# Kernel tuning notes

Measured on AMD Instinct MI355X. Metric: run time of the kernel, lower is better.

The kernel has to match this reference:

```python
import math
import jax, jax.numpy as jnp
import numpy as np

_GELU_C = math.sqrt(2.0 / math.pi)

def _gelu_tanh(x):
    return 0.5 * x * (1.0 + jnp.tanh(_GELU_C * (x + 0.044715 * x * x * x)))

def _l2_normalize(v, eps=1e-12):
    # matches F.normalize: v / max(||v||, eps)
    n = jnp.sqrt(jnp.sum(v * v, axis=-1, keepdims=True))
    return v / jnp.maximum(n, eps)

def setup_inputs() -> dict:
    key = jax.random.key(0)
    k1, k2, k3 = jax.random.split(key, 3)
    B, T, D = 8, 2048, 1024
    x = jax.random.normal(k1, (B, T, D), dtype=jnp.float32)
    # nn.Parameter initial values from the module
    log_alpha = jnp.asarray(math.log(math.exp(0.5) - 1.0), dtype=jnp.float32)
    log_sigma = jnp.asarray(math.log(1.0), dtype=jnp.float32)
    return {"x": x, "log_alpha": log_alpha, "log_sigma": log_sigma}

def reference(x, log_alpha, log_sigma):
    B, T, D = x.shape
    alpha = jax.nn.softplus(log_alpha)
    sigma = jax.nn.softplus(log_sigma)
    scale = 1.0 / math.sqrt(D)
    # full strictly-past causal attention (triu with diagonal=0 masks self too)
    sim = jnp.einsum('btd,bsd->bts', x, x) * scale            # [B,T,T]
    causal = jnp.triu(jnp.ones((T, T), dtype=bool), k=0)      # True = masked
    sim = jnp.where(causal[None], -jnp.inf, sim)
    # NaN-safe masked softmax: fully-masked rows (t=0) -> all zeros,
    # matching torch softmax + nan_to_num(nan=0.0)
    m = jnp.max(sim, axis=-1, keepdims=True)
    m_safe = jnp.where(jnp.isfinite(m), m, 0.0)
    e = jnp.exp(sim - m_safe)                                 # -inf -> 0
    denom = jnp.sum(e, axis=-1, keepdims=True)
    attn = jnp.where(denom > 0, e / jnp.where(denom > 0, denom, 1.0), 0.0)
    context = jnp.einsum('bts,bsd->btd', attn, x)             # [B,T,D]
    cos_sim = jnp.sum(_l2_normalize(x) * _l2_normalize(context), axis=-1)  # [B,T]
    novelty = jnp.clip(1.0 - cos_sim, 0.0, 2.0) / 2.0
    novelty = jnp.nan_to_num(novelty, nan=1.0)
    gate = 1.0 + alpha * jnp.tanh(sigma * novelty[..., None])
    return _gelu_tanh(x * gate)
```

## Files before the change

### kernel.cpp

```cpp
#include <hip/hip_runtime.h>
#include <math.h>

#define TN 2048
#define DN 1024

typedef __attribute__((ext_vector_type(8))) _Float16 half8;
typedef __attribute__((ext_vector_type(4))) _Float16 half4v;
typedef __attribute__((ext_vector_type(4))) float f32x4;

__device__ __forceinline__ f32x4 mfma16(half8 a, half8 b, f32x4 c) {
  return __builtin_amdgcn_mfma_f32_16x16x32_f16(a, b, c, 0, 0, 0);
}

#define BAR_LDS()  asm volatile("s_waitcnt lgkmcnt(0)\ns_barrier" ::: "memory")
#define WAITVM0()  asm volatile("s_waitcnt vmcnt(0)" ::: "memory")

__device__ __forceinline__ int img_off(int key, int f) {
  const int kg = key >> 2;
  const int p  = ((kg & 1) << 2) | (kg >> 1);
  return (f >> 4) * 512 + p * 64 + (key & 3) * 16 + (f & 15);
}

__global__ __launch_bounds__(256) void convert_x(const float* __restrict__ x,
                                                 _Float16* __restrict__ w) {
  const long long gid = (long long)blockIdx.x * 256 + threadIdx.x;
  const long long e   = gid * 8;
  const int bt   = (int)(e >> 15);
  const int et   = (int)(e & 32767);
  const int f16b = et >> 9;
  const int p    = (et >> 6) & 7;
  const int row  = (et >> 4) & 3;
  const int col0 = et & 15;
  const int kg   = ((p & 3) << 1) | (p >> 2);
  const int key  = kg * 4 + row;
  const size_t xoff = ((size_t)bt * 32 + key) * DN + f16b * 16 + col0;
  float4 u0 = *(const float4*)(x + xoff);
  float4 u1 = *(const float4*)(x + xoff + 4);
  half8 h = {(_Float16)u0.x, (_Float16)u0.y, (_Float16)u0.z, (_Float16)u0.w,
             (_Float16)u1.x, (_Float16)u1.y, (_Float16)u1.z, (_Float16)u1.w};
  *(half8*)(w + e) = h;
}

#define ISSUE4(T, O0, O1, O2, O3)                                             \
  asm volatile("ds_read_b64_tr_b16 %0, %4 offset:" O0 "\n\t"                  \
               "ds_read_b64_tr_b16 %1, %4 offset:" O1 "\n\t"                  \
               "ds_read_b64_tr_b16 %2, %4 offset:" O2 "\n\t"                  \
               "ds_read_b64_tr_b16 %3, %4 offset:" O3                         \
               : "=&v"(T[0]), "=&v"(T[1]), "=&v"(T[2]), "=&v"(T[3])           \
               : "v"(ab));

#define MFMA2(T, CT0, CT1)                                                    \
  {                                                                           \
    half8 bf0 = __builtin_shufflevector(T[0], T[1], 0, 1, 2, 3, 4, 5, 6, 7);  \
    half8 bf1 = __builtin_shufflevector(T[2], T[3], 0, 1, 2, 3, 4, 5, 6, 7);  \
    oacc[CT0] = mfma16(aP, bf0, oacc[CT0]);                                   \
    oacc[CT1] = mfma16(aP, bf1, oacc[CT1]);                                   \
  }

template <bool WS>
__global__ __launch_bounds__(512, 4)
void attn_gate(const float* __restrict__ x, const _Float16* __restrict__ wsx,
               const float* __restrict__ pla, const float* __restrict__ pls,
               float* __restrict__ out) {
  __shared__ _Float16 Kbuf[32768];
  __shared__ _Float16 Sred[8][16][40];
  __shared__ float l_s[16], gate_s[16];

  const int tid = threadIdx.x;
  const int w   = tid >> 6;
  const int l   = tid & 63;
  const int lr  = l & 15;
  const int lg  = l >> 4;
  const int kq  = w;

  const int b   = blockIdx.x & 7;
  const int q16 = 127 - (blockIdx.x >> 3);
  const int qbase = q16 * 16;
  const int nkt   = (qbase + 14) / 32 + 1;

  const float alpha = log1pf(expf(pla[0]));
  const float sigma = log1pf(expf(pls[0]));

  const float* xb = x + (size_t)b * TN * DN;
  float*       ob = out + (size_t)b * TN * DN;

  const int kg0 = lr >> 2;
  const int bk0 = ((((kg0 & 1) << 2) | (kg0 >> 1)) << 6) + (lr & 3) * 16 + (lg & 1) * 8;
  const int kg1 = 4 + (lr >> 2);
  const int bk1 = ((((kg1 & 1) << 2) | (kg1 >> 1)) << 6) + (lr & 3) * 16 + (lg & 1) * 8;

  auto STAGE = [&](int t) {
    if constexpr (WS) {
      const _Float16* tn = wsx + (size_t)(b * 64 + t) * 32768;
#pragma unroll
      for (int i = 0; i < 8; ++i)
        __builtin_amdgcn_global_load_lds(
            (const __attribute__((address_space(1))) void*)(tn + w * 4096 + i * 512 + l * 8),
            (__attribute__((address_space(3))) void*)(&Kbuf[w * 4096 + i * 512]), 16, 0, 0);
    } else {
      const int skey = tid >> 4, sc = tid & 15;
      const float* kp = xb + (size_t)(t * 32 + skey) * DN + sc * 4;
#pragma unroll
      for (int j = 0; j < 16; ++j) {
        const int f = sc * 4 + 64 * j;
        float4 v = *(const float4*)(kp + 64 * j);
        half4v h = {(_Float16)v.x, (_Float16)v.y, (_Float16)v.z, (_Float16)v.w};
        *(half4v*)&Kbuf[img_off(skey, f)] = h;
      }
    }
  };

  STAGE(0);

  half8 qf[4];
  if constexpr (WS) {
    const _Float16* qtile = wsx + (size_t)(b * 64 + (q16 >> 1)) * 32768;
    const int qrow = (q16 & 1) * 16 + lr;
    const int g0   = qrow >> 2;
    const int qp   = (((g0 & 1) << 2) | (g0 >> 1)) * 64 + (qrow & 3) * 16 + (lg & 1) * 8;
#pragma unroll
    for (int s = 0; s < 4; ++s)
      qf[s] = *(const half8*)&qtile[(kq * 8 + s * 2 + (lg >> 1)) * 512 + qp];
  } else {
#pragma unroll
    for (int s = 0; s < 4; ++s) {
      const float* qp = xb + (size_t)(qbase + lr) * DN + kq * 128 + s * 32 + lg * 8;
      float4 a = ((const float4*)qp)[0];
      float4 c = ((const float4*)qp)[1];
      half8 h;
      h[0]=(_Float16)a.x; h[1]=(_Float16)a.y; h[2]=(_Float16)a.z; h[3]=(_Float16)a.w;
      h[4]=(_Float16)c.x; h[5]=(_Float16)c.y; h[6]=(_Float16)c.z; h[7]=(_Float16)c.w;
      qf[s] = h;
    }
  }

  f32x4 oacc[8];
#pragma unroll
  for (int ct = 0; ct < 8; ++ct) oacc[ct] = f32x4{0.f, 0.f, 0.f, 0.f};
  float l0 = 0.0f;

  if constexpr (!WS) __syncthreads();

  for (int t = 0; t < nkt; ++t) {
    if constexpr (WS) WAITVM0();

    {
      f32x4 sA = f32x4{0.f,0.f,0.f,0.f};
      f32x4 sB = f32x4{0.f,0.f,0.f,0.f};
#pragma unroll
      for (int s = 0; s < 4; ++s) {
        const int base = (kq * 8 + s * 2 + (lg >> 1)) * 512;
        half8 bf0 = *(const half8*)&Kbuf[base + bk0];
        half8 bf1 = *(const half8*)&Kbuf[base + bk1];
        sA = mfma16(bf0, qf[s], sA);
        sB = mfma16(bf1, qf[s], sB);
      }
      half4v hA = {(_Float16)sA[0], (_Float16)sA[1], (_Float16)sA[2], (_Float16)sA[3]};
      half4v hB = {(_Float16)sB[0], (_Float16)sB[1], (_Float16)sB[2], (_Float16)sB[3]};
      *(half4v*)&Sred[kq][lr][lg * 4]      = hA;
      *(half4v*)&Sred[kq][lr][16 + lg * 4] = hB;
    }
    BAR_LDS();

    {
      half8 r0 = *(const half8*)&Sred[0][lr][lg * 8];
      half8 r1 = *(const half8*)&Sred[1][lr][lg * 8];
      half8 r2 = *(const half8*)&Sred[2][lr][lg * 8];
      half8 r3 = *(const half8*)&Sred[3][lr][lg * 8];
      half8 r4 = *(const half8*)&Sred[4][lr][lg * 8];
      half8 r5 = *(const half8*)&Sred[5][lr][lg * 8];
      half8 r6 = *(const half8*)&Sred[6][lr][lg * 8];
      half8 r7 = *(const half8*)&Sred[7][lr][lg * 8];
      half8 sum = ((r0 + r1) + (r2 + r3)) + ((r4 + r5) + (r6 + r7));

      const bool mt = (t == nkt - 1);
      const int  gb = 32 * t + lg * 8;
      half8 aP;
#pragma unroll
      for (int j = 0; j < 8; ++j) {
        float p = __expf((float)sum[j] * 0.03125f);
        if (mt && (gb + j >= qbase + lr)) p = 0.0f;
        l0 += p;
        aP[j] = (_Float16)p;
      }

      const uint32_t ab = (uint32_t)(uintptr_t)(void*)&Kbuf[w * 4096 + l * 4];
      asm volatile("s_waitcnt lgkmcnt(0)" ::: "memory");
      __builtin_amdgcn_sched_barrier(0);
      half4v t0[4], t1[4];
      ISSUE4(t0, "0", "512", "1024", "1536");
      ISSUE4(t1, "2048", "2560", "3072", "3584");
      asm volatile("s_waitcnt lgkmcnt(4)" ::: "memory");
      __builtin_amdgcn_sched_barrier(0);
      MFMA2(t0, 0, 1);
      ISSUE4(t0, "4096", "4608", "5120", "5632");
      asm volatile("s_waitcnt lgkmcnt(4)" ::: "memory");
      __builtin_amdgcn_sched_barrier(0);
      MFMA2(t1, 2, 3);
      ISSUE4(t1, "6144", "6656", "7168", "7680");
      asm volatile("s_waitcnt lgkmcnt(4)" ::: "memory");
      __builtin_amdgcn_sched_barrier(0);
      MFMA2(t0, 4, 5);
      asm volatile("s_waitcnt lgkmcnt(0)" ::: "memory");
      __builtin_amdgcn_sched_barrier(0);
      MFMA2(t1, 6, 7);
    }

    if (t + 1 < nkt) {
      if constexpr (!WS) __syncthreads();
      STAGE(t + 1);
    }
    BAR_LDS();
  }

  {
    float lt = l0 + __shfl_xor(l0, 16);
    lt += __shfl_xor(lt, 32);
    if (w == 0 && lg == 0) l_s[lr] = lt;
  }

  {
    float* ered = (float*)&Sred[0][0][0];
#pragma unroll
    for (int j = 0; j < 4; ++j) {
      const int row = lg * 4 + j;
      const float* xr = xb + (size_t)(qbase + row) * DN + w * 128 + lr;
      float a1 = 0.f, a2 = 0.f, a3 = 0.f;
#pragma unroll
      for (int ct = 0; ct < 8; ++ct) {
        const float xv = xr[ct * 16];
        const float ov = oacc[ct][j];
        a1 += xv * ov; a2 += xv * xv; a3 += ov * ov;
      }
#pragma unroll
      for (int d = 1; d < 16; d <<= 1) {
        a1 += __shfl_xor(a1, d);
        a2 += __shfl_xor(a2, d);
        a3 += __shfl_xor(a3, d);
      }
      if (lr == 0) {
        float* e = ered + (row * 8 + w) * 4;
        e[0] = a1; e[1] = a2; e[2] = a3;
      }
    }
  }
  __syncthreads();
  if (tid < 16) {
    const float* ered = (const float*)&Sred[0][0][0];
    float SxO = 0.f, Sxx = 0.f, SOO = 0.f;
#pragma unroll
    for (int wv = 0; wv < 8; ++wv) {
      const float* e = ered + (tid * 8 + wv) * 4;
      SxO += e[0]; Sxx += e[1]; SOO += e[2];
    }
    const float lden = l_s[tid];
    float cosv = 0.0f;
    if (lden > 0.0f) {
      const float nx = fmaxf(sqrtf(Sxx), 1e-12f);
      const float nc = fmaxf(sqrtf(SOO) / lden, 1e-12f);
      cosv = (SxO / lden) / (nx * nc);
    }
    float nov = fminf(fmaxf(1.0f - cosv, 0.0f), 2.0f) * 0.5f;
    gate_s[tid] = 1.0f + alpha * tanhf(sigma * nov);
  }
  __syncthreads();
  {
#pragma unroll
    for (int j = 0; j < 4; ++j) {
      const int row = lg * 4 + j;
      const float g = gate_s[row];
      const float* xr = xb + (size_t)(qbase + row) * DN + w * 128 + lr;
      float* orow     = ob + (size_t)(qbase + row) * DN + w * 128 + lr;
#pragma unroll
      for (int ct = 0; ct < 8; ++ct) {
        const float z = xr[ct * 16] * g;
        const float u = 0.7978845608028654f * (z + 0.044715f * z * z * z);
        orow[ct * 16] = 0.5f * z * (1.0f + tanhf(u));
      }
    }
  }
}

extern "C" void kernel_launch(void* const* d_in, const int* in_sizes, int n_in,
                              void* d_out, int out_size, void* d_ws, size_t ws_size,
                              hipStream_t stream) {
  const float* x  = (const float*)d_in[0];
  const float* la = (const float*)d_in[1];
  const float* ls = (const float*)d_in[2];
  float* out = (float*)d_out;
  const size_t need = (size_t)8 * 64 * 32768 * 2;
  if (ws_size >= need) {
    convert_x<<<dim3(8192), dim3(256), 0, stream>>>(x, (_Float16*)d_ws);
    attn_gate<true><<<dim3(1024), dim3(512), 0, stream>>>(
        x, (const _Float16*)d_ws, la, ls, out);
  } else {
    attn_gate<false><<<dim3(1024), dim3(512), 0, stream>>>(
        x, (const _Float16*)nullptr, la, ls, out);
  }
}
```

Before: 194.8 us.

## Load QK^T key fragments directly from global with one-tile register prefetch

In the workspace path, the key fragments for the score MFMA are now read directly from global memory into registers and prefetched one tile ahead, instead of being read from LDS after a full vmcnt(0) wait. The LDS-staged copy is still used only for the PV step, gated by a partial vmcnt(8) wait so the register prefetch loads can stay in flight. The Sred row pitch is also padded from 40 to 44 halves to change LDS bank mapping. The aim is to overlap global latency with compute and take traffic off LDS, at the cost of more VGPRs (16 half8 registers) and duplicated global reads that rely on cache hits.

```diff
diff --git a/kernel.cpp b/kernel.cpp
--- a/kernel.cpp
+++ b/kernel.cpp
@@ -13,7 +13,6 @@
 }
 
 #define BAR_LDS()  asm volatile("s_waitcnt lgkmcnt(0)\ns_barrier" ::: "memory")
-#define WAITVM0()  asm volatile("s_waitcnt vmcnt(0)" ::: "memory")
 
 __device__ __forceinline__ int img_off(int key, int f) {
   const int kg = key >> 2;
@@ -63,7 +62,7 @@
                const float* __restrict__ pla, const float* __restrict__ pls,
                float* __restrict__ out) {
   __shared__ _Float16 Kbuf[32768];
-  __shared__ _Float16 Sred[8][16][40];
+  __shared__ _Float16 Sred[8][16][44];
   __shared__ float l_s[16], gate_s[16];
 
   const int tid = threadIdx.x;
@@ -89,9 +88,11 @@
   const int kg1 = 4 + (lr >> 2);
   const int bk1 = ((((kg1 & 1) << 2) | (kg1 >> 1)) << 6) + (lr & 3) * 16 + (lg & 1) * 8;
 
+  const _Float16* wsb = WS ? (wsx + (size_t)b * 64 * 32768) : nullptr;
+
   auto STAGE = [&](int t) {
     if constexpr (WS) {
-      const _Float16* tn = wsx + (size_t)(b * 64 + t) * 32768;
+      const _Float16* tn = wsb + (size_t)t * 32768;
 #pragma unroll
       for (int i = 0; i < 8; ++i)
         __builtin_amdgcn_global_load_lds(
@@ -114,7 +115,7 @@
 
   half8 qf[4];
   if constexpr (WS) {
-    const _Float16* qtile = wsx + (size_t)(b * 64 + (q16 >> 1)) * 32768;
+    const _Float16* qtile = wsb + (size_t)(q16 >> 1) * 32768;
     const int qrow = (q16 & 1) * 16 + lr;
     const int g0   = qrow >> 2;
     const int qp   = (((g0 & 1) << 2) | (g0 >> 1)) * 64 + (qrow & 3) * 16 + (lg & 1) * 8;
@@ -134,6 +135,17 @@
     }
   }
 
+  half8 af0[4], af1[4];
+  if constexpr (WS) {
+    const _Float16* t0p = wsb;
+#pragma unroll
+    for (int s = 0; s < 4; ++s) {
+      const int base = (kq * 8 + s * 2 + (lg >> 1)) * 512;
+      af0[s] = *(const half8*)&t0p[base + bk0];
+      af1[s] = *(const half8*)&t0p[base + bk1];
+    }
+  }
+
   f32x4 oacc[8];
 #pragma unroll
   for (int ct = 0; ct < 8; ++ct) oacc[ct] = f32x4{0.f, 0.f, 0.f, 0.f};
@@ -142,23 +154,41 @@
   if constexpr (!WS) __syncthreads();
 
   for (int t = 0; t < nkt; ++t) {
-    if constexpr (WS) WAITVM0();
-
     {
       f32x4 sA = f32x4{0.f,0.f,0.f,0.f};
       f32x4 sB = f32x4{0.f,0.f,0.f,0.f};
-#pragma unroll
-      for (int s = 0; s < 4; ++s) {
-        const int base = (kq * 8 + s * 2 + (lg >> 1)) * 512;
-        half8 bf0 = *(const half8*)&Kbuf[base + bk0];
-        half8 bf1 = *(const half8*)&Kbuf[base + bk1];
-        sA = mfma16(bf0, qf[s], sA);
-        sB = mfma16(bf1, qf[s], sB);
+      if constexpr (WS) {
+#pragma unroll
+        for (int s = 0; s < 4; ++s) {
+          sA = mfma16(af0[s], qf[s], sA);
+          sB = mfma16(af1[s], qf[s], sB);
+        }
+      } else {
+#pragma unroll
+        for (int s = 0; s < 4; ++s) {
+          const int base = (kq * 8 + s * 2 + (lg >> 1)) * 512;
+          half8 bf0 = *(const half8*)&Kbuf[base + bk0];
+          half8 bf1 = *(const half8*)&Kbuf[base + bk1];
+          sA = mfma16(bf0, qf[s], sA);
+          sB = mfma16(bf1, qf[s], sB);
+        }
       }
       half4v hA = {(_Float16)sA[0], (_Float16)sA[1], (_Float16)sA[2], (_Float16)sA[3]};
       half4v hB = {(_Float16)sB[0], (_Float16)sB[1], (_Float16)sB[2], (_Float16)sB[3]};
       *(half4v*)&Sred[kq][lr][lg * 4]      = hA;
       *(half4v*)&Sred[kq][lr][16 + lg * 4] = hB;
+    }
+
+    if constexpr (WS) {
+      if (t + 1 < nkt) {
+        const _Float16* tn = wsb + (size_t)(t + 1) * 32768;
+#pragma unroll
+        for (int s = 0; s < 4; ++s) {
+          const int base = (kq * 8 + s * 2 + (lg >> 1)) * 512;
+          af0[s] = *(const half8*)&tn[base + bk0];
+          af1[s] = *(const half8*)&tn[base + bk1];
+        }
+      }
     }
     BAR_LDS();
 
@@ -186,6 +216,10 @@
 
       const uint32_t ab = (uint32_t)(uintptr_t)(void*)&Kbuf[w * 4096 + l * 4];
       asm volatile("s_waitcnt lgkmcnt(0)" ::: "memory");
+      if constexpr (WS) {
+        if (t + 1 < nkt) asm volatile("s_waitcnt vmcnt(8)" ::: "memory");
+        else             asm volatile("s_waitcnt vmcnt(0)" ::: "memory");
+      }
       __builtin_amdgcn_sched_barrier(0);
       half4v t0[4], t1[4];
       ISSUE4(t0, "0", "512", "1024", "1536");
```

After: 276.3 us. +41.9%, slower.
